# Optimization experiments

Measured on AMD Instinct MI355X. Metric: run time of the kernel, lower is better.

## Reference

```python
import jax, jax.numpy as jnp
import numpy as np

WIN = (9, 9)
EPS = 1e-05
DN = ('NCHW', 'OIHW', 'NCHW')


def _box_sum(x, win):
    # Separable box-sum (mathematically identical to conv2d with an all-ones
    kh = jnp.ones((1, 1, win[0], 1), x.dtype)
    kw = jnp.ones((1, 1, 1, win[1]), x.dtype)
    ph, pw = win[0] // 2, win[1] // 2
    x = jax.lax.conv_general_dilated(x, kh, (1, 1), [(ph, ph), (0, 0)], dimension_numbers=DN)
    x = jax.lax.conv_general_dilated(x, kw, (1, 1), [(0, 0), (pw, pw)], dimension_numbers=DN)
    return x


def setup_inputs() -> dict:
    key = jax.random.key(0)
    k1, k2 = jax.random.split(key)
    I = jax.random.normal(k1, (16, 1, 1024, 1024), dtype=jnp.float32)
    J = jax.random.normal(k2, (16, 1, 1024, 1024), dtype=jnp.float32)
    return {"I": I, "J": J}


def reference(I, J):
    win_size = WIN[0] * WIN[1]  # 81
    I_sum = _box_sum(I, WIN)
    J_sum = _box_sum(J, WIN)
    I2_sum = _box_sum(I * I, WIN)
    J2_sum = _box_sum(J * J, WIN)
    IJ_sum = _box_sum(I * J, WIN)

    u_I = I_sum / win_size
    u_J = J_sum / win_size

    cross = IJ_sum - u_J * I_sum - u_I * J_sum + u_I * u_J * win_size
    I_var = I2_sum - 2.0 * u_I * I_sum + u_I * u_I * win_size
    J_var = J2_sum - 2.0 * u_J * J_sum + u_J * u_J * win_size

    cc = cross * cross / (I_var * J_var + EPS)
    return -1.0 * jnp.mean(cc) + 1.0
```

## Files before the change

kernel.cpp:

```cpp
#include <hip/hip_runtime.h>

#define W_    1024
#define H_    1024
#define NIMG  16
#define HS    16
#define NTHR  256
#define PAD   4
#define EPS_  1e-5f
#define LDSW  1032

__device__ __forceinline__ float4 ldq(const float* p) {
    return *reinterpret_cast<const float4*>(p);
}
__device__ __forceinline__ float4 ldq_or0(const float* p, bool v) {
    return v ? *reinterpret_cast<const float4*>(p) : make_float4(0.f, 0.f, 0.f, 0.f);
}

__global__ __launch_bounds__(NTHR, 4) void ncc_main(const float* __restrict__ Iall,
                                                    const float* __restrict__ Jall,
                                                    float* __restrict__ acc)
{
    const int bx    = blockIdx.x;
    const int sbx   = (bx & 7) * 128 + (bx >> 3);
    const int img   = sbx >> 6;
    const int strip = sbx & 63;
    const int r0    = strip * HS;
    const int t     = threadIdx.x;
    const int c0    = t * 4;

    const float* __restrict__ Ib = Iall + (size_t)img * (W_ * H_) + c0;
    const float* __restrict__ Jb = Jall + (size_t)img * (W_ * H_) + c0;

    __shared__ float vs[5][LDSW];

    if (t < 8) {
        const int idx = (t < 4) ? t : (1024 + t);
        #pragma unroll
        for (int ch = 0; ch < 5; ++ch) vs[ch][idx] = 0.0f;
    }

    float vsum[5][4];
    #pragma unroll
    for (int ch = 0; ch < 5; ++ch)
        #pragma unroll
        for (int k = 0; k < 4; ++k) vsum[ch][k] = 0.f;

    for (int q = r0 - PAD; q < r0 + PAD; ++q) {
        if (q >= 0) {
            const float4 a = ldq(Ib + (size_t)q * W_);
            const float4 b = ldq(Jb + (size_t)q * W_);
            const float av[4] = {a.x, a.y, a.z, a.w};
            const float bv[4] = {b.x, b.y, b.z, b.w};
            #pragma unroll
            for (int k = 0; k < 4; ++k) {
                vsum[0][k] += av[k];
                vsum[1][k] += bv[k];
                vsum[2][k] = __builtin_fmaf(av[k], av[k], vsum[2][k]);
                vsum[3][k] = __builtin_fmaf(bv[k], bv[k], vsum[3][k]);
                vsum[4][k] = __builtin_fmaf(av[k], bv[k], vsum[4][k]);
            }
        }
    }

    float4 eI = ldq_or0(Ib + (size_t)(r0 + PAD) * W_, r0 + PAD < H_);
    float4 eJ = ldq_or0(Jb + (size_t)(r0 + PAD) * W_, r0 + PAD < H_);
    float4 lI = ldq_or0(Ib + (size_t)(r0 - PAD) * W_, r0 - PAD >= 0);
    float4 lJ = ldq_or0(Jb + (size_t)(r0 - PAD) * W_, r0 - PAD >= 0);

    float accum = 0.0f;
    const float inv81 = 1.0f / 81.0f;

    for (int r = r0; r < r0 + HS; ++r) {
        {
            const float av[4] = {eI.x, eI.y, eI.z, eI.w};
            const float bv[4] = {eJ.x, eJ.y, eJ.z, eJ.w};
            #pragma unroll
            for (int k = 0; k < 4; ++k) {
                vsum[0][k] += av[k];
                vsum[1][k] += bv[k];
                vsum[2][k] = __builtin_fmaf(av[k], av[k], vsum[2][k]);
                vsum[3][k] = __builtin_fmaf(bv[k], bv[k], vsum[3][k]);
                vsum[4][k] = __builtin_fmaf(av[k], bv[k], vsum[4][k]);
            }
        }
        #pragma unroll
        for (int ch = 0; ch < 5; ++ch)
            *reinterpret_cast<float4*>(&vs[ch][c0 + 4]) =
                make_float4(vsum[ch][0], vsum[ch][1], vsum[ch][2], vsum[ch][3]);
        __syncthreads();

        float4 L[5], R[5];
        #pragma unroll
        for (int ch = 0; ch < 5; ++ch) {
            L[ch] = ldq(&vs[ch][c0]);
            R[ch] = ldq(&vs[ch][c0 + 8]);
        }

        const float4 eI2 = ldq_or0(Ib + (size_t)(r + PAD + 1) * W_, r + PAD + 1 < H_);
        const float4 eJ2 = ldq_or0(Jb + (size_t)(r + PAD + 1) * W_, r + PAD + 1 < H_);
        const float4 lI2 = ldq_or0(Ib + (size_t)(r - PAD + 1) * W_, r - PAD + 1 >= 0);
        const float4 lJ2 = ldq_or0(Jb + (size_t)(r - PAD + 1) * W_, r - PAD + 1 >= 0);

        float h[5][4];
        #pragma unroll
        for (int ch = 0; ch < 5; ++ch) {
            float w[12];
            w[0] = L[ch].x; w[1] = L[ch].y; w[2]  = L[ch].z; w[3]  = L[ch].w;
            w[4] = vsum[ch][0]; w[5] = vsum[ch][1]; w[6] = vsum[ch][2]; w[7] = vsum[ch][3];
            w[8] = R[ch].x; w[9] = R[ch].y; w[10] = R[ch].z; w[11] = R[ch].w;
            float s = w[0];
            #pragma unroll
            for (int x = 1; x < 9; ++x) s += w[x];
            h[ch][0] = s;
            #pragma unroll
            for (int c = 1; c < 4; ++c) { s += w[c + 8] - w[c - 1]; h[ch][c] = s; }
        }
        #pragma unroll
        for (int c = 0; c < 4; ++c) {
            const float SI = h[0][c], SJ = h[1][c];
            const float SII = h[2][c], SJJ = h[3][c], SIJ = h[4][c];
            const float cross = __builtin_fmaf(-SI * SJ, inv81, SIJ);
            const float iv    = __builtin_fmaf(-SI * SI, inv81, SII);
            const float jv    = __builtin_fmaf(-SJ * SJ, inv81, SJJ);
            accum = __builtin_fmaf(cross * cross,
                                   __builtin_amdgcn_rcpf(__builtin_fmaf(iv, jv, EPS_)),
                                   accum);
        }

        {
            const float av[4] = {lI.x, lI.y, lI.z, lI.w};
            const float bv[4] = {lJ.x, lJ.y, lJ.z, lJ.w};
            #pragma unroll
            for (int k = 0; k < 4; ++k) {
                vsum[0][k] -= av[k];
                vsum[1][k] -= bv[k];
                vsum[2][k] = __builtin_fmaf(-av[k], av[k], vsum[2][k]);
                vsum[3][k] = __builtin_fmaf(-bv[k], bv[k], vsum[3][k]);
                vsum[4][k] = __builtin_fmaf(-av[k], bv[k], vsum[4][k]);
            }
        }
        __syncthreads();

        eI = eI2; eJ = eJ2; lI = lI2; lJ = lJ2;
    }

    #pragma unroll
    for (int off = 32; off > 0; off >>= 1) accum += __shfl_down(accum, off);
    if ((t & 63) == 0) atomicAdd(acc, accum);
}

__global__ void ncc_finalize(const float* __restrict__ acc, float* __restrict__ out)
{
    out[0] = 1.0f - acc[0] * (1.0f / (float)((size_t)NIMG * W_ * H_));
}

extern "C" void kernel_launch(void* const* d_in, const int* in_sizes, int n_in,
                              void* d_out, int out_size, void* d_ws, size_t ws_size,
                              hipStream_t stream)
{
    const float* I = (const float*)d_in[0];
    const float* J = (const float*)d_in[1];
    float* acc = (float*)d_ws;

    hipMemsetAsync(acc, 0, sizeof(float), stream);
    ncc_main<<<NIMG * (H_ / HS), NTHR, 0, stream>>>(I, J, acc);
    ncc_finalize<<<1, 1, 0, stream>>>(acc, (float*)d_out);
}
```

Baseline: 215.1 us.

## Split rows into single-wavefront column tiles with redundant halo sums to drop barriers

Each 1024-wide strip is now split into four 256-column tiles, each handled by a 64-thread block (one wavefront), so the __syncthreads barriers around the LDS exchange are removed. The edge lanes of each tile keep extra vertical sums for a 4-column halo, loading neighbouring columns redundantly. The software prefetch of the next row is dropped in favour of loading the current rows inside the loop. The aim is to avoid barrier stalls and raise occupancy, at the cost of extra halo loads, edge-lane divergence and less explicit load latency hiding. It also relies on implicit wavefront lockstep for the LDS write/read ordering.

Result: no change. 213.2 us (-0.9%).

```diff
diff --git a/kernel.cpp b/kernel.cpp
--- a/kernel.cpp
+++ b/kernel.cpp
@@ -1,13 +1,15 @@
 #include <hip/hip_runtime.h>
 
-#define W_    1024
-#define H_    1024
-#define NIMG  16
-#define HS    16
-#define NTHR  256
-#define PAD   4
-#define EPS_  1e-5f
-#define LDSW  1032
+#define W_     1024
+#define H_     1024
+#define NIMG   16
+#define HS     16
+#define PAD    4
+#define EPS_   1e-5f
+#define TILEC  256
+#define NTILE  (W_ / TILEC)
+#define NSTRIP (H_ / HS)
+#define NBLK   (NIMG * NSTRIP * NTILE)
 
 __device__ __forceinline__ float4 ldq(const float* p) {
     return *reinterpret_cast<const float4*>(p);
@@ -16,98 +18,109 @@
     return v ? *reinterpret_cast<const float4*>(p) : make_float4(0.f, 0.f, 0.f, 0.f);
 }
 
-__global__ __launch_bounds__(NTHR, 4) void ncc_main(const float* __restrict__ Iall,
-                                                    const float* __restrict__ Jall,
-                                                    float* __restrict__ acc)
+__device__ __forceinline__ void updA(float (&s)[5][4], const float4& a, const float4& b) {
+    const float av[4] = {a.x, a.y, a.z, a.w};
+    const float bv[4] = {b.x, b.y, b.z, b.w};
+    #pragma unroll
+    for (int k = 0; k < 4; ++k) {
+        s[0][k] += av[k];
+        s[1][k] += bv[k];
+        s[2][k] = __builtin_fmaf(av[k], av[k], s[2][k]);
+        s[3][k] = __builtin_fmaf(bv[k], bv[k], s[3][k]);
+        s[4][k] = __builtin_fmaf(av[k], bv[k], s[4][k]);
+    }
+}
+__device__ __forceinline__ void updS(float (&s)[5][4], const float4& a, const float4& b) {
+    const float av[4] = {a.x, a.y, a.z, a.w};
+    const float bv[4] = {b.x, b.y, b.z, b.w};
+    #pragma unroll
+    for (int k = 0; k < 4; ++k) {
+        s[0][k] -= av[k];
+        s[1][k] -= bv[k];
+        s[2][k] = __builtin_fmaf(-av[k], av[k], s[2][k]);
+        s[3][k] = __builtin_fmaf(-bv[k], bv[k], s[3][k]);
+        s[4][k] = __builtin_fmaf(-av[k], bv[k], s[4][k]);
+    }
+}
+
+__global__ __launch_bounds__(64) void ncc_main(const float* __restrict__ Iall,
+                                               const float* __restrict__ Jall,
+                                               float* __restrict__ acc)
 {
-    const int bx    = blockIdx.x;
-    const int sbx   = (bx & 7) * 128 + (bx >> 3);
-    const int img   = sbx >> 6;
-    const int strip = sbx & 63;
-    const int r0    = strip * HS;
-    const int t     = threadIdx.x;
-    const int c0    = t * 4;
+    const int bx  = blockIdx.x;
+    const int sbx = (bx & 7) * (NBLK / 8) + (bx >> 3);
+    const int tile  = sbx & (NTILE - 1);
+    const int strip = (sbx >> 2) & (NSTRIP - 1);
+    const int img   = sbx >> 8;
 
-    const float* __restrict__ Ib = Iall + (size_t)img * (W_ * H_) + c0;
-    const float* __restrict__ Jb = Jall + (size_t)img * (W_ * H_) + c0;
+    const int r0 = strip * HS;
+    const int C0 = tile * TILEC;
+    const int l  = threadIdx.x;
+    const int c0 = C0 + 4 * l;
 
-    __shared__ float vs[5][LDSW];
+    const float* __restrict__ Ib = Iall + (size_t)img * (W_ * H_);
+    const float* __restrict__ Jb = Jall + (size_t)img * (W_ * H_);
 
-    if (t < 8) {
-        const int idx = (t < 4) ? t : (1024 + t);
-        #pragma unroll
-        for (int ch = 0; ch < 5; ++ch) vs[ch][idx] = 0.0f;
-    }
+    __shared__ float vs[5][272];
 
-    float vsum[5][4];
-    #pragma unroll
-    for (int ch = 0; ch < 5; ++ch)
-        #pragma unroll
-        for (int k = 0; k < 4; ++k) vsum[ch][k] = 0.f;
+    const bool eL   = (l == 0);
+    const bool eR   = (l == 63);
+    const bool edge = eL || eR;
+    const bool hOwn = (eL && C0 > 0) || (eR && (C0 + TILEC) < W_);
+    const int  hc   = eL ? (C0 - 4) : (C0 + TILEC);
+
+    float vsum[5][4]  = {};
+    float vsumH[5][4] = {};
 
     for (int q = r0 - PAD; q < r0 + PAD; ++q) {
         if (q >= 0) {
-            const float4 a = ldq(Ib + (size_t)q * W_);
-            const float4 b = ldq(Jb + (size_t)q * W_);
-            const float av[4] = {a.x, a.y, a.z, a.w};
-            const float bv[4] = {b.x, b.y, b.z, b.w};
-            #pragma unroll
-            for (int k = 0; k < 4; ++k) {
-                vsum[0][k] += av[k];
-                vsum[1][k] += bv[k];
-                vsum[2][k] = __builtin_fmaf(av[k], av[k], vsum[2][k]);
-                vsum[3][k] = __builtin_fmaf(bv[k], bv[k], vsum[3][k]);
-                vsum[4][k] = __builtin_fmaf(av[k], bv[k], vsum[4][k]);
-            }
+            const size_t ro = (size_t)q * W_;
+            updA(vsum, ldq(Ib + ro + c0), ldq(Jb + ro + c0));
+            const float4 ah = ldq_or0(Ib + ro + hc, hOwn);
+            const float4 bh = ldq_or0(Jb + ro + hc, hOwn);
+            if (edge) updA(vsumH, ah, bh);
         }
     }
-
-    float4 eI = ldq_or0(Ib + (size_t)(r0 + PAD) * W_, r0 + PAD < H_);
-    float4 eJ = ldq_or0(Jb + (size_t)(r0 + PAD) * W_, r0 + PAD < H_);
-    float4 lI = ldq_or0(Ib + (size_t)(r0 - PAD) * W_, r0 - PAD >= 0);
-    float4 lJ = ldq_or0(Jb + (size_t)(r0 - PAD) * W_, r0 - PAD >= 0);
 
     float accum = 0.0f;
     const float inv81 = 1.0f / 81.0f;
 
     for (int r = r0; r < r0 + HS; ++r) {
-        {
-            const float av[4] = {eI.x, eI.y, eI.z, eI.w};
-            const float bv[4] = {eJ.x, eJ.y, eJ.z, eJ.w};
-            #pragma unroll
-            for (int k = 0; k < 4; ++k) {
-                vsum[0][k] += av[k];
-                vsum[1][k] += bv[k];
-                vsum[2][k] = __builtin_fmaf(av[k], av[k], vsum[2][k]);
-                vsum[3][k] = __builtin_fmaf(bv[k], bv[k], vsum[3][k]);
-                vsum[4][k] = __builtin_fmaf(av[k], bv[k], vsum[4][k]);
-            }
-        }
+        const int  qe  = r + PAD, ql = r - PAD;
+        const bool okE = qe < H_, okL = ql >= 0;
+        const size_t roE = (size_t)qe * W_, roL = (size_t)ql * W_;
+
+        const float4 eI  = ldq_or0(Ib + roE + c0, okE);
+        const float4 eJ  = ldq_or0(Jb + roE + c0, okE);
+        const float4 lI  = ldq_or0(Ib + roL + c0, okL);
+        const float4 lJ  = ldq_or0(Jb + roL + c0, okL);
+        const float4 eIh = ldq_or0(Ib + roE + hc, hOwn && okE);
+        const float4 eJh = ldq_or0(Jb + roE + hc, hOwn && okE);
+        const float4 lIh = ldq_or0(Ib + roL + hc, hOwn && okL);
+        const float4 lJh = ldq_or0(Jb + roL + hc, hOwn && okL);
+
+        updA(vsum, eI, eJ);
         #pragma unroll
         for (int ch = 0; ch < 5; ++ch)
-            *reinterpret_cast<float4*>(&vs[ch][c0 + 4]) =
+            *reinterpret_cast<float4*>(&vs[ch][4 + 4 * l]) =
                 make_float4(vsum[ch][0], vsum[ch][1], vsum[ch][2], vsum[ch][3]);
-        __syncthreads();
-
-        float4 L[5], R[5];
-        #pragma unroll
-        for (int ch = 0; ch < 5; ++ch) {
-            L[ch] = ldq(&vs[ch][c0]);
-            R[ch] = ldq(&vs[ch][c0 + 8]);
+        if (edge) {
+            updA(vsumH, eIh, eJh);
+            const int hidx = eL ? 0 : 260;
+            #pragma unroll
+            for (int ch = 0; ch < 5; ++ch)
+                *reinterpret_cast<float4*>(&vs[ch][hidx]) =
+                    make_float4(vsumH[ch][0], vsumH[ch][1], vsumH[ch][2], vsumH[ch][3]);
         }
-
-        const float4 eI2 = ldq_or0(Ib + (size_t)(r + PAD + 1) * W_, r + PAD + 1 < H_);
-        const float4 eJ2 = ldq_or0(Jb + (size_t)(r + PAD + 1) * W_, r + PAD + 1 < H_);
-        const float4 lI2 = ldq_or0(Ib + (size_t)(r - PAD + 1) * W_, r - PAD + 1 >= 0);
-        const float4 lJ2 = ldq_or0(Jb + (size_t)(r - PAD + 1) * W_, r - PAD + 1 >= 0);
 
         float h[5][4];
         #pragma unroll
         for (int ch = 0; ch < 5; ++ch) {
-            float w[12];
-            w[0] = L[ch].x; w[1] = L[ch].y; w[2]  = L[ch].z; w[3]  = L[ch].w;
-            w[4] = vsum[ch][0]; w[5] = vsum[ch][1]; w[6] = vsum[ch][2]; w[7] = vsum[ch][3];
-            w[8] = R[ch].x; w[9] = R[ch].y; w[10] = R[ch].z; w[11] = R[ch].w;
+            const float4 Lq = ldq(&vs[ch][4 * l]);
+            const float4 Rq = ldq(&vs[ch][4 * l + 8]);
+            const float w[12] = {Lq.x, Lq.y, Lq.z, Lq.w,
+                                 vsum[ch][0], vsum[ch][1], vsum[ch][2], vsum[ch][3],
+                                 Rq.x, Rq.y, Rq.z, Rq.w};
             float s = w[0];
             #pragma unroll
             for (int x = 1; x < 9; ++x) s += w[x];
@@ -127,26 +140,13 @@
                                    accum);
         }
 
-        {
-            const float av[4] = {lI.x, lI.y, lI.z, lI.w};
-            const float bv[4] = {lJ.x, lJ.y, lJ.z, lJ.w};
-            #pragma unroll
-            for (int k = 0; k < 4; ++k) {
-                vsum[0][k] -= av[k];
-                vsum[1][k] -= bv[k];
-                vsum[2][k] = __builtin_fmaf(-av[k], av[k], vsum[2][k]);
-                vsum[3][k] = __builtin_fmaf(-bv[k], bv[k], vsum[3][k]);
-                vsum[4][k] = __builtin_fmaf(-av[k], bv[k], vsum[4][k]);
-            }
-        }
-        __syncthreads();
-
-        eI = eI2; eJ = eJ2; lI = lI2; lJ = lJ2;
+        updS(vsum, lI, lJ);
+        if (edge) updS(vsumH, lIh, lJh);
     }
 
     #pragma unroll
     for (int off = 32; off > 0; off >>= 1) accum += __shfl_down(accum, off);
-    if ((t & 63) == 0) atomicAdd(acc, accum);
+    if (l == 0) atomicAdd(acc, accum);
 }
 
 __global__ void ncc_finalize(const float* __restrict__ acc, float* __restrict__ out)
@@ -163,6 +163,6 @@
     float* acc = (float*)d_ws;
 
     hipMemsetAsync(acc, 0, sizeof(float), stream);
-    ncc_main<<<NIMG * (H_ / HS), NTHR, 0, stream>>>(I, J, acc);
+    ncc_main<<<NBLK, 64, 0, stream>>>(I, J, acc);
     ncc_finalize<<<1, 1, 0, stream>>>(acc, (float*)d_out);
 }
```
